# Optimization experiments

Measured on AMD Instinct MI355X. Metric: run time of the kernel, lower is better.

The kernel has to match this reference:

```python
import jax, jax.numpy as jnp
import numpy as np

B, N, DIM, H, DH = 2, 2048, 1024, 16, 64
ALPHA = 32.0 ** 2  # stable_softmax alpha
SCALE = DH ** -0.5


def rotate_half(x):
    # interleaved pairs: (x0, x1, x2, x3, ...) -> (-x1, x0, -x3, x2, ...)
    xp = x.reshape(x.shape[:-1] + (-1, 2))
    return jnp.stack((-xp[..., 1], xp[..., 0]), axis=-1).reshape(x.shape)


def apply_rotary(freqs, t):
    # freqs: [n, d]; t: [b, h, n, d]
    return t * jnp.cos(freqs) + rotate_half(t) * jnp.sin(freqs)


def setup_inputs() -> dict:
    key = jax.random.key(0)
    k0, k1, k2, k3 = jax.random.split(key, 4)
    x = jax.random.normal(k0, (B, N, DIM), jnp.float32)
    rotary_pos_emb = jax.random.normal(k1, (N, DH), jnp.float32)
    w_qkv = jax.random.normal(k2, (DIM, 3 * H * DH), jnp.float32) / np.sqrt(DIM)
    w_out = jax.random.normal(k3, (H * DH, DIM), jnp.float32) / np.sqrt(H * DH)
    b_out = jnp.zeros((DIM,), jnp.float32)
    return {"x": x, "rotary_pos_emb": rotary_pos_emb, "w_qkv": w_qkv,
            "w_out": w_out, "b_out": b_out}


def reference(x, rotary_pos_emb, w_qkv, w_out, b_out):
    b, n, _ = x.shape
    qkv = x @ w_qkv                                  # [b, n, 3*h*d]
    q, k, v = jnp.split(qkv, 3, axis=-1)
    to_heads = lambda t: t.reshape(b, n, H, DH).transpose(0, 2, 1, 3)  # [b,h,n,d]
    q, k, v = map(to_heads, (q, k, v))
    freqs = rotary_pos_emb[:n]
    # source applies rotary emb to q, k AND v
    q = apply_rotary(freqs, q)
    k = apply_rotary(freqs, k)
    v = apply_rotary(freqs, v)
    q = q * SCALE
    dots = jnp.einsum('bhid,bhjd->bhij', q, k)       # [b,h,n,n]
    mask_value = -jnp.finfo(dots.dtype).max
    causal = jnp.triu(jnp.ones((n, n), bool), 1)
    dots = jnp.where(causal, mask_value, dots)
    # stable softmax: divide by alpha, subtract detached max, rescale
    t = dots / ALPHA
    t = t - jax.lax.stop_gradient(jnp.max(t, axis=-1, keepdims=True))
    attn = jax.nn.softmax(t * ALPHA, axis=-1)
    out = jnp.einsum('bhij,bhjd->bhid', attn, v)     # [b,h,n,d]
    out = out.transpose(0, 2, 1, 3).reshape(b, n, H * DH)
    return out @ w_out + b_out
```

## Files before the change

### kernel.cpp

```cpp
#include <hip/hip_runtime.h>
#include <stdint.h>

#define DEV __device__ __forceinline__

typedef __bf16 bf16x8 __attribute__((ext_vector_type(8)));
typedef float  f32x4  __attribute__((ext_vector_type(4)));
typedef short  s16x8  __attribute__((ext_vector_type(8)));

constexpr int Bb   = 2;
constexpr int Nn   = 2048;
constexpr int DIMc = 1024;
constexpr int Hh   = 16;
constexpr int DHc  = 64;
constexpr int BN   = Bb * Nn;
constexpr int QKVC = 3 * Hh * DHc;

DEV ushort f2b(float f) {
  uint32_t u = __float_as_uint(f);
  u += 0x7fffu + ((u >> 16) & 1u);
  return (ushort)(u >> 16);
}

DEV void gload16(const void* g, void* l) {
  __builtin_amdgcn_global_load_lds(
      (const __attribute__((address_space(1))) void*)(uintptr_t)g,
      (__attribute__((address_space(3))) void*)(uint32_t)(uintptr_t)l,
      16, 0, 0);
}

DEV f32x4 mfma16(bf16x8 a, bf16x8 b, f32x4 c) {
  return __builtin_amdgcn_mfma_f32_16x16x32_bf16(a, b, c, 0, 0, 0);
}

DEV uint32_t cvtpk(float lo, float hi) {
  uint32_t r;
  asm("v_cvt_pk_bf16_f32 %0, %1, %2" : "=v"(r) : "v"(lo), "v"(hi));
  return r;
}


__global__ void k_cast_x(const float* __restrict__ x, ushort* __restrict__ xb,
                         const float* __restrict__ rope, float2* __restrict__ csT) {
  int i = blockIdx.x * 256 + threadIdx.x;
  size_t base = (size_t)i * 8;
  s16x8 v;
#pragma unroll
  for (int j = 0; j < 8; ++j) v[j] = (short)f2b(x[base + j]);
  *(s16x8*)(xb + base) = v;
  if (i < Nn * DHc) {
    float t = rope[i];
    float s, c;
    sincosf(t, &s, &c);
    csT[i] = make_float2(c, s);
  }
}

__global__ void k_transpose_cast(const float* __restrict__ src, ushort* __restrict__ dst,
                                 int K, int Ncols) {
  __shared__ float tile[32][33];
  int nb = blockIdx.x * 32, kb = blockIdx.y * 32;
  int tx = threadIdx.x, ty = threadIdx.y;
#pragma unroll
  for (int i = 0; i < 4; ++i) {
    int k = ty + i * 8;
    tile[k][tx] = src[(size_t)(kb + k) * Ncols + nb + tx];
  }
  __syncthreads();
#pragma unroll
  for (int i = 0; i < 4; ++i) {
    int n = ty + i * 8;
    dst[(size_t)(nb + n) * K + kb + tx] = f2b(tile[tx][n]);
  }
}

DEV void gemm_core(const ushort* __restrict__ A, const ushort* __restrict__ Bt,
                   int rowBase, int colBase, ushort* lA, ushort* lB,
                   f32x4 (&acc)[4][4]) {
  const int tid = threadIdx.x;
  const int lane = tid & 63, w = tid >> 6;
  const int wm = w >> 1, wn = w & 1;
  const int g = lane >> 4, l16 = lane & 15;
  const f32x4 zero = {0.f, 0.f, 0.f, 0.f};
#pragma unroll
  for (int i = 0; i < 4; ++i)
#pragma unroll
    for (int j = 0; j < 4; ++j) acc[i][j] = zero;

  const int c0row = tid >> 2,          c0kc = (tid & 3) ^ ((c0row >> 1) & 3);
  const int c1row = (256 + tid) >> 2,  c1kc = (tid & 3) ^ ((c1row >> 1) & 3);
  const ushort* gA0 = A  + (size_t)(rowBase + c0row) * DIMc + c0kc * 8;
  const ushort* gA1 = A  + (size_t)(rowBase + c1row) * DIMc + c1kc * 8;
  const ushort* gB0 = Bt + (size_t)(colBase + c0row) * DIMc + c0kc * 8;
  const ushort* gB1 = Bt + (size_t)(colBase + c1row) * DIMc + c1kc * 8;
  const size_t o0 = (size_t)(0 * 256 + w * 64) * 8;
  const size_t o1 = (size_t)(1 * 256 + w * 64) * 8;
  constexpr int BUF = 128 * 32;

  gload16(gA0,      lA + o0);        gload16(gB0,      lB + o0);
  gload16(gA1,      lA + o1);        gload16(gB1,      lB + o1);
  gload16(gA0 + 32, lA + BUF + o0);  gload16(gB0 + 32, lB + BUF + o0);
  gload16(gA1 + 32, lA + BUF + o1);  gload16(gB1 + 32, lB + BUF + o1);
  asm volatile("s_waitcnt vmcnt(4)" ::: "memory");
  __builtin_amdgcn_s_barrier();

  int cur = 0;
  for (int k0 = 0; k0 < DIMc; k0 += 32) {
    const ushort* cA = lA + cur * BUF;
    const ushort* cB = lB + cur * BUF;

    bf16x8 af[4], bfr[4];
#pragma unroll
    for (int f = 0; f < 4; ++f) {
      int r  = wm * 64 + f * 16 + l16;
      int r2 = wn * 64 + f * 16 + l16;
      af[f]  = *(const bf16x8*)&cA[r  * 32 + ((g ^ ((r  >> 1) & 3)) << 3)];
      bfr[f] = *(const bf16x8*)&cB[r2 * 32 + ((g ^ ((r2 >> 1) & 3)) << 3)];
    }

    const int kn = k0 + 64;
    if (kn < DIMc) {
      int st = cur + 2; if (st >= 3) st -= 3;
      ushort* nA = lA + st * BUF;
      ushort* nB = lB + st * BUF;
      gload16(gA0 + kn, nA + o0);  gload16(gB0 + kn, nB + o0);
      gload16(gA1 + kn, nA + o1);  gload16(gB1 + kn, nB + o1);
    }

#pragma unroll
    for (int i = 0; i < 4; ++i)
#pragma unroll
      for (int j = 0; j < 4; ++j)
        acc[i][j] = mfma16(af[i], bfr[j], acc[i][j]);

    if (kn < DIMc) {
      asm volatile("s_waitcnt vmcnt(4)" ::: "memory");
    } else if (k0 + 32 < DIMc) {
      asm volatile("s_waitcnt vmcnt(0)" ::: "memory");
    }
    asm volatile("s_waitcnt lgkmcnt(0)" ::: "memory");
    __builtin_amdgcn_s_barrier();
    cur += 1; if (cur == 3) cur = 0;
  }
}

__global__ __launch_bounds__(256) void k_gemm_qkv(
    const ushort* __restrict__ xb, const ushort* __restrict__ wT,
    const float2* __restrict__ csT,
    ushort* __restrict__ Qd, ushort* __restrict__ Kd, ushort* __restrict__ Vd) {
  __shared__ ushort lA[3 * 128 * 32];
  __shared__ ushort lB[3 * 128 * 32];
  f32x4 acc[4][4];
  const int rowBase = blockIdx.y * 128, colBase = blockIdx.x * 128;
  gemm_core(xb, wT, rowBase, colBase, lA, lB, acc);

  const int lane = threadIdx.x & 63, w = threadIdx.x >> 6;
  const int wm = w >> 1, wn = w & 1;
  const int g = lane >> 4, l16 = lane & 15;
#pragma unroll
  for (int fm = 0; fm < 4; ++fm) {
#pragma unroll
    for (int fn = 0; fn < 4; ++fn) {
      int col = colBase + wn * 64 + fn * 16 + l16;
      int sel = col >> 10, hc = col & 1023;
      int h = hc >> 6, d = hc & 63;
      float sgn = (d & 1) ? 1.f : -1.f;
#pragma unroll
      for (int r = 0; r < 4; ++r) {
        float t  = acc[fm][fn][r];
        float tp = __shfl_xor(t, 1);
        int row = rowBase + wm * 64 + fm * 16 + 4 * g + r;
        int b = row >> 11, n = row & 2047;
        float2 cs = csT[n * 64 + d];
        float rv = t * cs.x + sgn * tp * cs.y;
        if (sel == 0) {
          Qd[((size_t)(b * Hh + h) * Nn + n) * DHc + d] = f2b(rv * 0.125f);
        } else if (sel == 1) {
          Kd[((size_t)(b * Hh + h) * Nn + n) * DHc + d] = f2b(rv);
        } else {
          Vd[((size_t)(b * Hh + h) * DHc + d) * Nn + n] = f2b(rv);
        }
      }
    }
  }
}


DEV void stageKV(const ushort* __restrict__ Kh, const ushort* __restrict__ Vh,
                 ushort* lKb, ushort* lVb, int kt, int tid, int w) {
#pragma unroll
  for (int s = 0; s < 2; ++s) {
    int c = s * 256 + tid;
    int row = c >> 3, jst = c & 7;
    int jl = jst ^ (row & 7);
    gload16(Kh + (size_t)(kt * 64 + row) * DHc + jl * 8,
            lKb + (size_t)(s * 256 + w * 64) * 8);
    gload16(Vh + (size_t)row * Nn + kt * 64 + jl * 8,
            lVb + (size_t)(s * 256 + w * 64) * 8);
  }
}

DEV void attn_step(const ushort* lKc, const ushort* lVc, char* lPw,
                   const bf16x8 (&q)[2], f32x4 (&o)[4], float& m, float& l,
                   int kBase, int qg, bool diag, int g, int l16) {
  const f32x4 zero = {0.f, 0.f, 0.f, 0.f};
  f32x4 s[4];
#pragma unroll
  for (int jt = 0; jt < 4; ++jt) s[jt] = zero;

#pragma unroll
  for (int jt = 0; jt < 4; ++jt) {
    int jr = jt * 16 + l16;
#pragma unroll
    for (int d0 = 0; d0 < 2; ++d0) {
      bf16x8 kb = *(const bf16x8*)&lKc[jr * 64 + (((d0 * 4 + g) ^ (jr & 7)) << 3)];
      s[jt] = mfma16(kb, q[d0], s[jt]);
    }
  }

  if (diag) {
#pragma unroll
    for (int jt = 0; jt < 4; ++jt)
#pragma unroll
      for (int r = 0; r < 4; ++r) {
        int j = kBase + jt * 16 + 4 * g + r;
        if (j > qg) s[jt][r] = -3.0e38f;
      }
  }

  float tmax = fmaxf(fmaxf(fmaxf(s[0][0], s[0][1]), fmaxf(s[0][2], s[0][3])),
                     fmaxf(fmaxf(s[1][0], s[1][1]), fmaxf(s[1][2], s[1][3])));
  tmax = fmaxf(tmax, fmaxf(fmaxf(fmaxf(s[2][0], s[2][1]), fmaxf(s[2][2], s[2][3])),
                           fmaxf(fmaxf(s[3][0], s[3][1]), fmaxf(s[3][2], s[3][3]))));
  tmax = fmaxf(tmax, __shfl_xor(tmax, 16));
  tmax = fmaxf(tmax, __shfl_xor(tmax, 32));

  if (!__all(tmax <= m + 8.f)) {
    float mnew = fmaxf(m, tmax);
    float sc = __expf(m - mnew);
#pragma unroll
    for (int dt = 0; dt < 4; ++dt) o[dt] *= sc;
    l *= sc;
    m = mnew;
  }

  float ps = 0.f;
#pragma unroll
  for (int jt = 0; jt < 4; ++jt)
#pragma unroll
    for (int r = 0; r < 4; ++r) {
      float p = __expf(s[jt][r] - m);
      s[jt][r] = p;
      ps += p;
    }
  ps += __shfl_xor(ps, 16);
  ps += __shfl_xor(ps, 32);
  l += ps;

  const int sw = (l16 & 7) << 4;
  char* prow = lPw + l16 * 128;
#pragma unroll
  for (int jt = 0; jt < 4; ++jt) {
    int jo = (jt * 16 + 4 * g) * 2;
    *(uint32_t*)(prow + (jo ^ sw))       = cvtpk(s[jt][0], s[jt][1]);
    *(uint32_t*)(prow + ((jo + 4) ^ sw)) = cvtpk(s[jt][2], s[jt][3]);
  }

  bf16x8 pa[2];
#pragma unroll
  for (int jh = 0; jh < 2; ++jh)
    pa[jh] = *(const bf16x8*)(prow + (((jh * 32 + 8 * g) * 2) ^ sw));
#pragma unroll
  for (int dt = 0; dt < 4; ++dt) {
    int d = dt * 16 + l16;
#pragma unroll
    for (int jh = 0; jh < 2; ++jh) {
      bf16x8 vb = *(const bf16x8*)&lVc[d * 64 + (((jh * 4 + g) ^ (d & 7)) << 3)];
      o[dt] = mfma16(vb, pa[jh], o[dt]);
    }
  }
}

DEV void attn_epi(ushort* __restrict__ ao, int bh, int n, int g,
                  f32x4 (&o)[4], float l) {
  const int b = bh >> 4, h = bh & 15;
  float inv = 1.f / l;
  ushort* dst = ao + (size_t)(b * Nn + n) * (Hh * DHc) + h * 64;
#pragma unroll
  for (int dt = 0; dt < 4; ++dt) {
    uint2 pkd;
    pkd.x = cvtpk(o[dt][0] * inv, o[dt][1] * inv);
    pkd.y = cvtpk(o[dt][2] * inv, o[dt][3] * inv);
    *(uint2*)(dst + dt * 16 + 4 * g) = pkd;
  }
}

__global__ __launch_bounds__(256) void k_attn(
    const ushort* __restrict__ Qd, const ushort* __restrict__ Kd,
    const ushort* __restrict__ Vd, ushort* __restrict__ ao) {
  __shared__ ushort lK[2][64 * 64];
  __shared__ ushort lV[2][64 * 64];
  __shared__ char   lP[4][16 * 128];
  const int tid = threadIdx.x;
  const int lane = tid & 63, w = tid >> 6;
  const int g = lane >> 4, l16 = lane & 15;
  const int bh = blockIdx.y;
  const int p = blockIdx.x;
  const int tA = p, tB = 31 - p;
  const int last = tB;
  const ushort* Qh = Qd + (size_t)bh * Nn * DHc;
  const ushort* Kh = Kd + (size_t)bh * Nn * DHc;
  const ushort* Vh = Vd + (size_t)bh * DHc * Nn;

  const int qgA = tA * 64 + w * 16 + l16;
  const int qgB = tB * 64 + w * 16 + l16;

  bf16x8 qA[2], qB[2];
#pragma unroll
  for (int d0 = 0; d0 < 2; ++d0) {
    qA[d0] = *(const bf16x8*)(Qh + (size_t)qgA * DHc + d0 * 32 + g * 8);
    qB[d0] = *(const bf16x8*)(Qh + (size_t)qgB * DHc + d0 * 32 + g * 8);
  }

  const f32x4 zero = {0.f, 0.f, 0.f, 0.f};
  f32x4 oA[4], oB[4];
#pragma unroll
  for (int dt = 0; dt < 4; ++dt) { oA[dt] = zero; oB[dt] = zero; }
  float mA = -3.0e38f, lA_ = 0.f, mB = -3.0e38f, lB_ = 0.f;

  stageKV(Kh, Vh, lK[0], lV[0], 0, tid, w);

  for (int kt = 0; kt <= last; ++kt) {
    const int cur = kt & 1;
    if (kt < last) {
      stageKV(Kh, Vh, lK[cur ^ 1], lV[cur ^ 1], kt + 1, tid, w);
      asm volatile("s_waitcnt vmcnt(4)" ::: "memory");
    } else {
      asm volatile("s_waitcnt vmcnt(0)" ::: "memory");
    }
    __builtin_amdgcn_s_barrier();

    attn_step(lK[cur], lV[cur], lP[w], qB, oB, mB, lB_, kt * 64, qgB, kt == tB, g, l16);
    if (kt <= tA)
      attn_step(lK[cur], lV[cur], lP[w], qA, oA, mA, lA_, kt * 64, qgA, kt == tA, g, l16);

    __builtin_amdgcn_s_barrier();
  }

  attn_epi(ao, bh, qgA, g, oA, lA_);
  attn_epi(ao, bh, qgB, g, oB, lB_);
}

__global__ __launch_bounds__(256) void k_gemm_out(
    const ushort* __restrict__ ao, const ushort* __restrict__ wT,
    const float* __restrict__ bias, float* __restrict__ out) {
  __shared__ ushort lA[3 * 64 * 32];
  __shared__ ushort lB[3 * 128 * 32];
  const int tid = threadIdx.x;
  const int lane = tid & 63, w = tid >> 6;
  const int g = lane >> 4, l16 = lane & 15;
  const int rowBase = blockIdx.y * 64, colBase = blockIdx.x * 128;

  f32x4 acc[4][2];
  const f32x4 zero = {0.f, 0.f, 0.f, 0.f};
#pragma unroll
  for (int i = 0; i < 4; ++i) { acc[i][0] = zero; acc[i][1] = zero; }

  const int arow = tid >> 2, akc = (tid & 3) ^ ((arow >> 1) & 3);
  const int b1row = 64 + arow, b1kc = (tid & 3) ^ ((b1row >> 1) & 3);
  const ushort* gA  = ao + (size_t)(rowBase + arow) * DIMc + akc * 8;
  const ushort* gB0 = wT + (size_t)(colBase + arow) * DIMc + akc * 8;
  const ushort* gB1 = wT + (size_t)(colBase + b1row) * DIMc + b1kc * 8;
  const size_t oA  = (size_t)w * 512;
  const size_t oB0 = (size_t)w * 512;
  const size_t oB1 = 2048 + (size_t)w * 512;
  constexpr int BUFA = 64 * 32, BUFB = 128 * 32;

  gload16(gA,      lA + oA);         gload16(gB0,      lB + oB0);         gload16(gB1,      lB + oB1);
  gload16(gA + 32, lA + BUFA + oA);  gload16(gB0 + 32, lB + BUFB + oB0);  gload16(gB1 + 32, lB + BUFB + oB1);
  asm volatile("s_waitcnt vmcnt(3)" ::: "memory");
  __builtin_amdgcn_s_barrier();

  int cur = 0;
  for (int k0 = 0; k0 < DIMc; k0 += 32) {
    const ushort* cA = lA + cur * BUFA;
    const ushort* cB = lB + cur * BUFB;

    bf16x8 af[4], bfr[2];
#pragma unroll
    for (int f = 0; f < 4; ++f) {
      int r = f * 16 + l16;
      af[f] = *(const bf16x8*)&cA[r * 32 + ((g ^ ((r >> 1) & 3)) << 3)];
    }
#pragma unroll
    for (int f = 0; f < 2; ++f) {
      int r2 = w * 32 + f * 16 + l16;
      bfr[f] = *(const bf16x8*)&cB[r2 * 32 + ((g ^ ((r2 >> 1) & 3)) << 3)];
    }

    const int kn = k0 + 64;
    if (kn < DIMc) {
      int st = cur + 2; if (st >= 3) st -= 3;
      gload16(gA + kn,  lA + st * BUFA + oA);
      gload16(gB0 + kn, lB + st * BUFB + oB0);
      gload16(gB1 + kn, lB + st * BUFB + oB1);
    }

#pragma unroll
    for (int i = 0; i < 4; ++i)
#pragma unroll
      for (int j = 0; j < 2; ++j)
        acc[i][j] = mfma16(af[i], bfr[j], acc[i][j]);

    if (kn < DIMc) {
      asm volatile("s_waitcnt vmcnt(3)" ::: "memory");
    } else if (k0 + 32 < DIMc) {
      asm volatile("s_waitcnt vmcnt(0)" ::: "memory");
    }
    asm volatile("s_waitcnt lgkmcnt(0)" ::: "memory");
    __builtin_amdgcn_s_barrier();
    cur += 1; if (cur == 3) cur = 0;
  }

#pragma unroll
  for (int fm = 0; fm < 4; ++fm)
#pragma unroll
    for (int fn = 0; fn < 2; ++fn) {
      int col = colBase + w * 32 + fn * 16 + l16;
#pragma unroll
      for (int r = 0; r < 4; ++r) {
        int row = rowBase + fm * 16 + 4 * g + r;
        out[(size_t)row * DIMc + col] = acc[fm][fn][r] + bias[col];
      }
    }
}

extern "C" void kernel_launch(void* const* d_in, const int* in_sizes, int n_in,
                              void* d_out, int out_size, void* d_ws, size_t ws_size,
                              hipStream_t stream) {
  const float* x     = (const float*)d_in[0];
  const float* rope  = (const float*)d_in[1];
  const float* w_qkv = (const float*)d_in[2];
  const float* w_out = (const float*)d_in[3];
  const float* b_out = (const float*)d_in[4];
  float* out = (float*)d_out;

  char* ws = (char*)d_ws;
  ushort* xb    = (ushort*)(ws);
  ushort* wqkvT = (ushort*)(ws + 8388608);
  ushort* woutT = (ushort*)(ws + 14680064);
  float2* csT   = (float2*)(ws + 16777216);
  ushort* Qd    = (ushort*)(ws + 17825792);
  ushort* Kd    = (ushort*)(ws + 26214400);
  ushort* Vd    = (ushort*)(ws + 34603008);
  ushort* ao    = (ushort*)(ws + 42991616);

  hipLaunchKernelGGL(k_cast_x, dim3(2048), dim3(256), 0, stream, x, xb, rope, csT);
  hipLaunchKernelGGL(k_transpose_cast, dim3(QKVC / 32, DIMc / 32), dim3(32, 8), 0, stream,
                     w_qkv, wqkvT, DIMc, QKVC);
  hipLaunchKernelGGL(k_transpose_cast, dim3(DIMc / 32, DIMc / 32), dim3(32, 8), 0, stream,
                     w_out, woutT, DIMc, DIMc);
  hipLaunchKernelGGL(k_gemm_qkv, dim3(QKVC / 128, BN / 128), dim3(256), 0, stream,
                     xb, wqkvT, csT, Qd, Kd, Vd);
  hipLaunchKernelGGL(k_attn, dim3(16, Bb * Hh), dim3(256), 0, stream, Qd, Kd, Vd, ao);
  hipLaunchKernelGGL(k_gemm_out, dim3(DIMc / 128, BN / 64), dim3(256), 0, stream,
                     ao, woutT, b_out, out);
}
```

Measured before the change: 130.4 us.

## Widen QKV GEMM tile to 128x256 with per-fragment B loads

The QKV projection GEMM now computes a 128x256 output tile per block instead of 128x128. Each wave holds a 4x8 accumulator grid, streams B fragments one at a time, and reuses the A fragments across eight MFMAs. The aim is to cut LDS and global traffic per FLOP and raise arithmetic intensity. In exchange it uses more registers and LDS and launches half as many blocks (384 instead of 768), which may reduce occupancy and wave-level parallelism on the CUs.

```diff
diff --git a/kernel.cpp b/kernel.cpp
--- a/kernel.cpp
+++ b/kernel.cpp
@@ -73,67 +73,76 @@
   }
 }
 
-DEV void gemm_core(const ushort* __restrict__ A, const ushort* __restrict__ Bt,
-                   int rowBase, int colBase, ushort* lA, ushort* lB,
-                   f32x4 (&acc)[4][4]) {
+__global__ __launch_bounds__(256, 2) void k_gemm_qkv(
+    const ushort* __restrict__ xb, const ushort* __restrict__ wT,
+    const float2* __restrict__ csT,
+    ushort* __restrict__ Qd, ushort* __restrict__ Kd, ushort* __restrict__ Vd) {
+  __shared__ ushort lA[3 * 128 * 32];
+  __shared__ ushort lB[3 * 256 * 32];
   const int tid = threadIdx.x;
   const int lane = tid & 63, w = tid >> 6;
   const int wm = w >> 1, wn = w & 1;
   const int g = lane >> 4, l16 = lane & 15;
+  const int rowBase = blockIdx.y * 128, colBase = blockIdx.x * 256;
+  constexpr int BUFA = 128 * 32, BUFB = 256 * 32;
+
+  f32x4 acc[4][8];
   const f32x4 zero = {0.f, 0.f, 0.f, 0.f};
 #pragma unroll
   for (int i = 0; i < 4; ++i)
 #pragma unroll
-    for (int j = 0; j < 4; ++j) acc[i][j] = zero;
-
-  const int c0row = tid >> 2,          c0kc = (tid & 3) ^ ((c0row >> 1) & 3);
-  const int c1row = (256 + tid) >> 2,  c1kc = (tid & 3) ^ ((c1row >> 1) & 3);
-  const ushort* gA0 = A  + (size_t)(rowBase + c0row) * DIMc + c0kc * 8;
-  const ushort* gA1 = A  + (size_t)(rowBase + c1row) * DIMc + c1kc * 8;
-  const ushort* gB0 = Bt + (size_t)(colBase + c0row) * DIMc + c0kc * 8;
-  const ushort* gB1 = Bt + (size_t)(colBase + c1row) * DIMc + c1kc * 8;
-  const size_t o0 = (size_t)(0 * 256 + w * 64) * 8;
-  const size_t o1 = (size_t)(1 * 256 + w * 64) * 8;
-  constexpr int BUF = 128 * 32;
-
-  gload16(gA0,      lA + o0);        gload16(gB0,      lB + o0);
-  gload16(gA1,      lA + o1);        gload16(gB1,      lB + o1);
-  gload16(gA0 + 32, lA + BUF + o0);  gload16(gB0 + 32, lB + BUF + o0);
-  gload16(gA1 + 32, lA + BUF + o1);  gload16(gB1 + 32, lB + BUF + o1);
-  asm volatile("s_waitcnt vmcnt(4)" ::: "memory");
+    for (int j = 0; j < 8; ++j) acc[i][j] = zero;
+
+  const int srow = tid >> 2;
+  const int skc  = (tid & 3) ^ ((srow >> 1) & 3);
+  const ushort* gA0 = xb + (size_t)(rowBase + srow) * DIMc + skc * 8;
+  const ushort* gB0 = wT + (size_t)(colBase + srow) * DIMc + skc * 8;
+  const size_t lo = (size_t)(w * 64) * 8;
+
+#pragma unroll
+  for (int t = 0; t < 2; ++t) {
+    gload16(gA0 + t * 32,              lA + t * BUFA + lo);
+    gload16(gA0 + 64 * DIMc + t * 32,  lA + t * BUFA + 2048 + lo);
+#pragma unroll
+    for (int s = 0; s < 4; ++s)
+      gload16(gB0 + (size_t)s * 64 * DIMc + t * 32, lB + t * BUFB + s * 2048 + lo);
+  }
+  asm volatile("s_waitcnt vmcnt(6)" ::: "memory");
   __builtin_amdgcn_s_barrier();
 
   int cur = 0;
   for (int k0 = 0; k0 < DIMc; k0 += 32) {
-    const ushort* cA = lA + cur * BUF;
-    const ushort* cB = lB + cur * BUF;
-
-    bf16x8 af[4], bfr[4];
+    const ushort* cA = lA + cur * BUFA;
+    const ushort* cB = lB + cur * BUFB;
+
+    bf16x8 aF[4];
 #pragma unroll
     for (int f = 0; f < 4; ++f) {
-      int r  = wm * 64 + f * 16 + l16;
-      int r2 = wn * 64 + f * 16 + l16;
-      af[f]  = *(const bf16x8*)&cA[r  * 32 + ((g ^ ((r  >> 1) & 3)) << 3)];
-      bfr[f] = *(const bf16x8*)&cB[r2 * 32 + ((g ^ ((r2 >> 1) & 3)) << 3)];
+      int r = wm * 64 + f * 16 + l16;
+      aF[f] = *(const bf16x8*)&cA[r * 32 + ((g ^ ((r >> 1) & 3)) << 3)];
     }
 
     const int kn = k0 + 64;
     if (kn < DIMc) {
       int st = cur + 2; if (st >= 3) st -= 3;
-      ushort* nA = lA + st * BUF;
-      ushort* nB = lB + st * BUF;
-      gload16(gA0 + kn, nA + o0);  gload16(gB0 + kn, nB + o0);
-      gload16(gA1 + kn, nA + o1);  gload16(gB1 + kn, nB + o1);
-    }
-
-#pragma unroll
-    for (int i = 0; i < 4; ++i)
-#pragma unroll
-      for (int j = 0; j < 4; ++j)
-        acc[i][j] = mfma16(af[i], bfr[j], acc[i][j]);
+      gload16(gA0 + kn,             lA + st * BUFA + lo);
+      gload16(gA0 + 64 * DIMc + kn, lA + st * BUFA + 2048 + lo);
+#pragma unroll
+      for (int s = 0; s < 4; ++s)
+        gload16(gB0 + (size_t)s * 64 * DIMc + kn, lB + st * BUFB + s * 2048 + lo);
+    }
+
+#pragma unroll
+    for (int nf = 0; nf < 8; ++nf) {
+      int r2 = wn * 128 + nf * 16 + l16;
+      bf16x8 bF = *(const bf16x8*)&cB[r2 * 32 + ((g ^ ((r2 >> 1) & 3)) << 3)];
+#pragma unroll
+      for (int mf = 0; mf < 4; ++mf)
+        acc[mf][nf] = mfma16(aF[mf], bF, acc[mf][nf]);
+    }
 
     if (kn < DIMc) {
-      asm volatile("s_waitcnt vmcnt(4)" ::: "memory");
+      asm volatile("s_waitcnt vmcnt(6)" ::: "memory");
     } else if (k0 + 32 < DIMc) {
       asm volatile("s_waitcnt vmcnt(0)" ::: "memory");
     }
@@ -141,26 +150,12 @@
     __builtin_amdgcn_s_barrier();
     cur += 1; if (cur == 3) cur = 0;
   }
-}
-
-__global__ __launch_bounds__(256) void k_gemm_qkv(
-    const ushort* __restrict__ xb, const ushort* __restrict__ wT,
-    const float2* __restrict__ csT,
-    ushort* __restrict__ Qd, ushort* __restrict__ Kd, ushort* __restrict__ Vd) {
-  __shared__ ushort lA[3 * 128 * 32];
-  __shared__ ushort lB[3 * 128 * 32];
-  f32x4 acc[4][4];
-  const int rowBase = blockIdx.y * 128, colBase = blockIdx.x * 128;
-  gemm_core(xb, wT, rowBase, colBase, lA, lB, acc);
-
-  const int lane = threadIdx.x & 63, w = threadIdx.x >> 6;
-  const int wm = w >> 1, wn = w & 1;
-  const int g = lane >> 4, l16 = lane & 15;
+
 #pragma unroll
   for (int fm = 0; fm < 4; ++fm) {
 #pragma unroll
-    for (int fn = 0; fn < 4; ++fn) {
-      int col = colBase + wn * 64 + fn * 16 + l16;
+    for (int fn = 0; fn < 8; ++fn) {
+      int col = colBase + wn * 128 + fn * 16 + l16;
       int sel = col >> 10, hc = col & 1023;
       int h = hc >> 6, d = hc & 63;
       float sgn = (d & 1) ? 1.f : -1.f;
@@ -459,7 +454,7 @@
                      w_qkv, wqkvT, DIMc, QKVC);
   hipLaunchKernelGGL(k_transpose_cast, dim3(DIMc / 32, DIMc / 32), dim3(32, 8), 0, stream,
                      w_out, woutT, DIMc, DIMc);
-  hipLaunchKernelGGL(k_gemm_qkv, dim3(QKVC / 128, BN / 128), dim3(256), 0, stream,
+  hipLaunchKernelGGL(k_gemm_qkv, dim3(QKVC / 256, BN / 128), dim3(256), 0, stream,
                      xb, wqkvT, csT, Qd, Kd, Vd);
   hipLaunchKernelGGL(k_attn, dim3(16, Bb * Hh), dim3(256), 0, stream, Qd, Kd, Vd, ao);
   hipLaunchKernelGGL(k_gemm_out, dim3(DIMc / 128, BN / 64), dim3(256), 0, stream,
```

Result: slower. 137.5 us (+5.4%).
